# Kernel tuning notes

Measured on AMD Instinct MI355X. Metric: run time of the kernel, lower is better.

The kernel has to match this reference:

```python
import jax, jax.numpy as jnp
import numpy as np
import math

HIDDEN = 1024
NUM_HEADS = 16
HEAD_DIM = HIDDEN // NUM_HEADS
B, S = 4, 1024


def setup_inputs() -> dict:
    key = jax.random.key(0)
    ks = jax.random.split(key, 16)
    sd = 1.0 / math.sqrt(HIDDEN)
    inp = {
        "x": jax.random.normal(ks[0], (B, S, HIDDEN), jnp.float32),
        "spikes": jax.random.uniform(ks[1], (B, S, HIDDEN), jnp.float32),
        "membrane_potential": jax.random.normal(ks[2], (B, S, HIDDEN), jnp.float32),
        "Wq": jax.random.normal(ks[3], (HIDDEN, HIDDEN), jnp.float32) * sd,
        "bq": jnp.zeros((HIDDEN,), jnp.float32),
        "Wk": jax.random.normal(ks[4], (HIDDEN, HIDDEN), jnp.float32) * sd,
        "bk": jnp.zeros((HIDDEN,), jnp.float32),
        "Wv": jax.random.normal(ks[5], (HIDDEN, HIDDEN), jnp.float32) * sd,
        "bv": jnp.zeros((HIDDEN,), jnp.float32),
        "Wo": jax.random.normal(ks[6], (HIDDEN, HIDDEN), jnp.float32) * sd,
        "bo": jnp.zeros((HIDDEN,), jnp.float32),
        "tau_decay": jnp.ones((NUM_HEADS,), jnp.float32) * 10.0,
        "Wg": jax.random.normal(ks[7], (HIDDEN, 2 * HIDDEN), jnp.float32) * sd,
        "bg": jnp.zeros((HIDDEN,), jnp.float32),
    }
    return inp


def _heads(t):  # [B,S,H] -> [B,nH,S,hd]
    Bv, Sv, _ = t.shape
    return t.reshape(Bv, Sv, NUM_HEADS, HEAD_DIM).transpose(0, 2, 1, 3)


def reference(x, spikes, membrane_potential, Wq, bq, Wk, bk, Wv, bv, Wo, bo, tau_decay, Wg, bg):
    scale = 1.0 / math.sqrt(HEAD_DIM)
    q = _heads(x @ Wq.T + bq)
    k = _heads(x @ Wk.T + bk)
    v = _heads(x @ Wv.T + bv)

    # raw scores [B,nH,S,S]
    scores = jnp.einsum('bhqd,bhkd->bhqk', q, k) * scale

    # per-head exponential temporal decay mask [nH,S,S]
    times = jnp.arange(S, dtype=jnp.float32)
    tdiff = jnp.abs(times[:, None] - times[None, :])  # [S,S]
    tmask = jnp.exp(-tdiff[None] / tau_decay[:, None, None])
    scores = scores * tmask[None]

    # spike correlation term
    sm = _heads(spikes)
    spike_attn = jnp.einsum('bhqd,bhkd->bhqk', sm, sm) * scale
    scores = scores * (1.0 + spike_attn)

    # membrane gating of V
    v = v * jax.nn.sigmoid(_heads(membrane_potential))

    probs = jax.nn.softmax(scores, axis=-1)
    context = jnp.einsum('bhqk,bhkd->bhqd', probs, v)
    context = context.transpose(0, 2, 1, 3).reshape(B, S, HIDDEN)

    # dendritic gate
    gate_in = jnp.concatenate([context, membrane_potential], axis=-1)
    gate = jax.nn.sigmoid(gate_in @ Wg.T + bg)
    context = context * gate

    return context @ Wo.T + bo
```

## Files before the change

### kernel.cpp

```cpp
#include <hip/hip_runtime.h>
#include <math.h>
#include <stdint.h>

namespace {

typedef __attribute__((ext_vector_type(8))) short s8v;
typedef __attribute__((ext_vector_type(4))) float f4v;
typedef unsigned short u16;

__device__ __forceinline__ float fexp2(float x) {
  return __builtin_amdgcn_exp2f(x);
}

__device__ __forceinline__ u16 f2bf(float f) {
  union { float f; uint32_t u; } v; v.f = f;
  uint32_t r = v.u + 0x7fffu + ((v.u >> 16) & 1u);
  return (u16)(r >> 16);
}
__device__ __forceinline__ float bf2f(u16 h) {
  union { uint32_t u; float f; } v; v.u = ((uint32_t)h) << 16;
  return v.f;
}
__device__ __forceinline__ uint32_t pk2r(float a, float b) {
  return (uint32_t)f2bf(a) | ((uint32_t)f2bf(b) << 16);
}
__device__ __forceinline__ uint32_t pk2(float a, float b) {
  union { float f; uint32_t u; } x, y; x.f = a; y.f = b;
  return ((x.u + 0x8000u) >> 16) | ((y.u + 0x8000u) & 0xffff0000u);
}
__device__ __forceinline__ float sigmoidf_(float x) { return 1.0f / (1.0f + __expf(-x)); }

__device__ __forceinline__ void gload16(const u16* g, u16* l) {
  __builtin_amdgcn_global_load_lds(
      (const __attribute__((address_space(1))) void*)g,
      (__attribute__((address_space(3))) void*)l, 16, 0, 0);
}

struct CvtJob { const float* src; u16* dst; };
struct CvtArgs { CvtJob j[18]; float* vz; };

__global__ __launch_bounds__(256) void cvt_kernel(CvtArgs a) {
  if (blockIdx.y == 0 && blockIdx.x < 4) {
    float4 z; z.x = 0.f; z.y = 0.f; z.z = 0.f; z.w = 0.f;
    ((float4*)a.vz)[blockIdx.x * 256 + threadIdx.x] = z;
  }
  const CvtJob jb = a.j[blockIdx.y];
  const int i = blockIdx.x * 256 + threadIdx.x;
  const float4 v = ((const float4*)jb.src)[i];
  uint2 pk;
  pk.x = pk2r(v.x, v.y);
  pk.y = pk2r(v.z, v.w);
  ((uint2*)jb.dst)[i] = pk;
}

__global__ __launch_bounds__(256) void qkv_gemm(
    const u16* __restrict__ xb,
    const u16* __restrict__ Wqb, const u16* __restrict__ Wkb, const u16* __restrict__ Wvb,
    const float* __restrict__ bq, const float* __restrict__ bk, const float* __restrict__ bv,
    const float* __restrict__ mem,
    u16* __restrict__ Qb, u16* __restrict__ Kb, u16* __restrict__ Vt,
    float* __restrict__ Vtot) {
  __shared__ __align__(16) u16 as_[2][4096], bs_[2][4096];
  const int t = threadIdx.x;
  const int nb = blockIdx.x, mb = blockIdx.y;
  const int sel = nb >> 3;
  const u16* W = sel == 0 ? Wqb : (sel == 1 ? Wkb : Wvb);
  const float* bias = sel == 0 ? bq : (sel == 1 ? bk : bv);
  const int m0 = mb * 128, n0 = (nb & 7) * 128;
  const f4v fz = {0.f, 0.f, 0.f, 0.f};
  f4v acc[4][4];
#pragma unroll
  for (int i = 0; i < 4; ++i)
#pragma unroll
    for (int j = 0; j < 4; ++j) acc[i][j] = fz;

  const int l = t & 63, w = t >> 6, wm = w >> 1, wn = w & 1;
  const int lr = l & 15, lq = l >> 4;
  const int rh = lr >> 1;
  const int rb4 = (lr & 1) << 2;

  const int sc0 = (t & 7) ^ ((t >> 3) & 7);
  const int sgrow = ((t >> 3) << 1) + (sc0 >> 2);
  const int sgk = (sc0 & 3) << 3;

#define QKV_STAGE(k0, bsel)                                                    \
  {                                                                            \
    const int kk_ = (k0);                                                      \
    _Pragma("unroll") for (int u = 0; u < 2; ++u) {                            \
      gload16(xb + (size_t)(m0 + u * 64 + sgrow) * 1024 + kk_ + sgk,           \
              &as_[bsel][u * 2048 + t * 8]);                                   \
      gload16(W + (size_t)(n0 + u * 64 + sgrow) * 1024 + kk_ + sgk,            \
              &bs_[bsel][u * 2048 + t * 8]);                                   \
    }                                                                          \
  }

  QKV_STAGE(0, 0);
  QKV_STAGE(32, 1);
  asm volatile("s_waitcnt vmcnt(4)" ::: "memory");
  __builtin_amdgcn_s_barrier();

  if (sel < 2) {
    for (int c = 0; c < 32; ++c) {
      const int pp = c & 1;
      s8v af[4], bf[4];
#pragma unroll
      for (int mi = 0; mi < 4; ++mi)
        af[mi] = *(const s8v*)(&as_[pp][(wm * 32 + mi * 8 + rh) * 64 +
                                        (((rb4 + lq) ^ rh) * 8)]);
#pragma unroll
      for (int ni = 0; ni < 4; ++ni)
        bf[ni] = *(const s8v*)(&bs_[pp][(wn * 32 + ni * 8 + rh) * 64 +
                                        (((rb4 + lq) ^ rh) * 8)]);
      asm volatile("s_waitcnt lgkmcnt(0)" ::: "memory");
      __builtin_amdgcn_sched_barrier(0);
      __builtin_amdgcn_s_barrier();
      if (c + 2 < 32) QKV_STAGE((c + 2) << 5, pp);
      __builtin_amdgcn_s_setprio(1);
#pragma unroll
      for (int mi = 0; mi < 4; ++mi)
#pragma unroll
        for (int ni = 0; ni < 4; ++ni)
          acc[mi][ni] = __builtin_amdgcn_mfma_f32_16x16x32_bf16(
              bf[ni], af[mi], acc[mi][ni], 0, 0, 0);
      __builtin_amdgcn_s_setprio(0);
      if (c + 2 < 32) {
        asm volatile("s_waitcnt vmcnt(4)" ::: "memory");
      } else if (c + 1 < 32) {
        asm volatile("s_waitcnt vmcnt(0)" ::: "memory");
      }
      if (c + 1 < 32) __builtin_amdgcn_s_barrier();
    }
    __builtin_amdgcn_sched_barrier(0);
    u16* dst = (sel == 0) ? Qb : Kb;
#pragma unroll
    for (int mi = 0; mi < 4; ++mi)
#pragma unroll
      for (int ni = 0; ni < 4; ++ni) {
        const int m = m0 + wm * 64 + mi * 16 + lr;
        const int nb4 = n0 + wn * 64 + ni * 16 + lq * 4;
        const float4 b4 = *(const float4*)&bias[nb4];
        uint2 pk;
        pk.x = pk2r(acc[mi][ni][0] + b4.x, acc[mi][ni][1] + b4.y);
        pk.y = pk2r(acc[mi][ni][2] + b4.z, acc[mi][ni][3] + b4.w);
        *(uint2*)(dst + (size_t)m * 1024 + nb4) = pk;
      }
  } else {
    for (int c = 0; c < 32; ++c) {
      const int pp = c & 1;
      s8v af[4], bf[4];
#pragma unroll
      for (int mi = 0; mi < 4; ++mi)
        af[mi] = *(const s8v*)(&as_[pp][(wm * 32 + mi * 8 + rh) * 64 +
                                        (((rb4 + lq) ^ rh) * 8)]);
#pragma unroll
      for (int ni = 0; ni < 4; ++ni)
        bf[ni] = *(const s8v*)(&bs_[pp][(wn * 32 + ni * 8 + rh) * 64 +
                                        (((rb4 + lq) ^ rh) * 8)]);
      asm volatile("s_waitcnt lgkmcnt(0)" ::: "memory");
      __builtin_amdgcn_sched_barrier(0);
      __builtin_amdgcn_s_barrier();
      if (c + 2 < 32) QKV_STAGE((c + 2) << 5, pp);
      __builtin_amdgcn_s_setprio(1);
#pragma unroll
      for (int mi = 0; mi < 4; ++mi)
#pragma unroll
        for (int ni = 0; ni < 4; ++ni)
          acc[mi][ni] = __builtin_amdgcn_mfma_f32_16x16x32_bf16(
              af[mi], bf[ni], acc[mi][ni], 0, 0, 0);
      __builtin_amdgcn_s_setprio(0);
      if (c + 2 < 32) {
        asm volatile("s_waitcnt vmcnt(4)" ::: "memory");
      } else if (c + 1 < 32) {
        asm volatile("s_waitcnt vmcnt(0)" ::: "memory");
      }
      if (c + 1 < 32) __builtin_amdgcn_s_barrier();
    }
    __builtin_amdgcn_sched_barrier(0);
    const int b = m0 >> 10;
    float vpart[4] = {0.f, 0.f, 0.f, 0.f};
#pragma unroll
    for (int mi = 0; mi < 4; ++mi)
#pragma unroll
      for (int ni = 0; ni < 4; ++ni) {
        const int mrow = m0 + wm * 64 + mi * 16 + lq * 4;
        const int ncol = n0 + wn * 64 + ni * 16 + lr;
        const int h = ncol >> 6, d = ncol & 63;
        const float bi = bias[ncol];
        float tv[4];
#pragma unroll
        for (int r = 0; r < 4; ++r)
          tv[r] = (acc[mi][ni][r] + bi) * sigmoidf_(mem[(size_t)(mrow + r) * 1024 + ncol]);
        vpart[ni] += (tv[0] + tv[1]) + (tv[2] + tv[3]);
        const int s = mrow & 1023;
        uint2 pk;
        pk.x = pk2r(tv[0], tv[1]);
        pk.y = pk2r(tv[2], tv[3]);
        *(uint2*)(Vt + ((size_t)((b * 16 + h) * 64 + d)) * 1024 + s) = pk;
      }
#pragma unroll
    for (int ni = 0; ni < 4; ++ni) {
      const int ncol = n0 + wn * 64 + ni * 16 + lr;
      atomicAdd(&Vtot[(size_t)(b * 16 + (ncol >> 6)) * 64 + (ncol & 63)], vpart[ni]);
    }
  }
#undef QKV_STAGE
}

template <int MODE>
__global__ __launch_bounds__(256) void gemm64(
    const u16* __restrict__ Ab, const u16* __restrict__ A2b,
    const u16* __restrict__ W, const float* __restrict__ bias,
    u16* __restrict__ outb, float* __restrict__ outf, int K) {
  __shared__ __align__(16) u16 as_[8192], bs_[16384];
  const int t = threadIdx.x, l = t & 63, w = t >> 6;
  const int wm = w >> 1, wn = w & 1, lr = l & 15, lq = l >> 4;
  const int m0 = blockIdx.y * 64, n0 = blockIdx.x * 128;
  const f4v fz = {0.f, 0.f, 0.f, 0.f};
  f4v acc[2][4];
#pragma unroll
  for (int i = 0; i < 2; ++i)
#pragma unroll
    for (int j = 0; j < 4; ++j) acc[i][j] = fz;
  const int rx = lr & 7;
  const int srow = t >> 3;
  const int scol = ((t & 7) ^ (srow & 7)) * 8;
  const int nc = K >> 6;

#define G64_STAGE(k0, bsel)                                                    \
  {                                                                            \
    const int kk_ = (k0);                                                      \
    const u16* Ae_ = Ab;                                                       \
    int ka_ = kk_;                                                             \
    if (MODE == 1 && kk_ >= 1024) { Ae_ = A2b; ka_ = kk_ - 1024; }             \
    _Pragma("unroll") for (int u = 0; u < 2; ++u)                              \
        gload16(Ae_ + (size_t)(m0 + u * 32 + srow) * 1024 + ka_ + scol,        \
                as_ + (bsel) * 4096 + u * 2048 + t * 8);                       \
    _Pragma("unroll") for (int u = 0; u < 4; ++u)                              \
        gload16(W + (size_t)(n0 + u * 32 + srow) * K + kk_ + scol,             \
                bs_ + (bsel) * 8192 + u * 2048 + t * 8);                       \
  }

  G64_STAGE(0, 0);
  G64_STAGE(64, 1);
  asm volatile("s_waitcnt vmcnt(6)" ::: "memory");
  __builtin_amdgcn_s_barrier();

  for (int c = 0; c < nc; ++c) {
    const int pp = c & 1;
    const int loA = pp * 4096, loB = pp * 8192;
    s8v af[2][2], bf[2][4];
#pragma unroll
    for (int ks = 0; ks < 2; ++ks) {
      const int co = ((ks * 4 + lq) ^ rx) * 8;
#pragma unroll
      for (int mi = 0; mi < 2; ++mi)
        af[ks][mi] = *(const s8v*)(as_ + loA + (wm * 32 + mi * 16 + lr) * 64 + co);
#pragma unroll
      for (int ni = 0; ni < 4; ++ni)
        bf[ks][ni] = *(const s8v*)(bs_ + loB + (wn * 64 + ni * 16 + lr) * 64 + co);
    }
    asm volatile("s_waitcnt lgkmcnt(0)" ::: "memory");
    __builtin_amdgcn_sched_barrier(0);
    __builtin_amdgcn_s_barrier();
    if (c + 2 < nc) G64_STAGE((c + 2) << 6, pp);
    __builtin_amdgcn_s_setprio(1);
#pragma unroll
    for (int ks = 0; ks < 2; ++ks)
#pragma unroll
      for (int mi = 0; mi < 2; ++mi)
#pragma unroll
        for (int ni = 0; ni < 4; ++ni)
          acc[mi][ni] = __builtin_amdgcn_mfma_f32_16x16x32_bf16(
              bf[ks][ni], af[ks][mi], acc[mi][ni], 0, 0, 0);
    __builtin_amdgcn_s_setprio(0);
    if (c + 2 < nc) {
      asm volatile("s_waitcnt vmcnt(6)" ::: "memory");
    } else if (c + 1 < nc) {
      asm volatile("s_waitcnt vmcnt(0)" ::: "memory");
    }
    if (c + 1 < nc) __builtin_amdgcn_s_barrier();
  }
  __builtin_amdgcn_sched_barrier(0);
#undef G64_STAGE

#pragma unroll
  for (int mi = 0; mi < 2; ++mi)
#pragma unroll
    for (int ni = 0; ni < 4; ++ni) {
      const int m = m0 + wm * 32 + mi * 16 + lr;
      const int nb4 = n0 + wn * 64 + ni * 16 + lq * 4;
      const float4 b4 = *(const float4*)&bias[nb4];
      if (MODE == 0) {
        float4 o;
        o.x = acc[mi][ni][0] + b4.x; o.y = acc[mi][ni][1] + b4.y;
        o.z = acc[mi][ni][2] + b4.z; o.w = acc[mi][ni][3] + b4.w;
        *(float4*)(outf + (size_t)m * 1024 + nb4) = o;
      } else {
        const uint2 a2 = *(const uint2*)(Ab + (size_t)m * 1024 + nb4);
        float cx[4] = {bf2f((u16)(a2.x & 0xffff)), bf2f((u16)(a2.x >> 16)),
                       bf2f((u16)(a2.y & 0xffff)), bf2f((u16)(a2.y >> 16))};
        float g[4];
        g[0] = cx[0] * sigmoidf_(acc[mi][ni][0] + b4.x);
        g[1] = cx[1] * sigmoidf_(acc[mi][ni][1] + b4.y);
        g[2] = cx[2] * sigmoidf_(acc[mi][ni][2] + b4.z);
        g[3] = cx[3] * sigmoidf_(acc[mi][ni][3] + b4.w);
        uint2 pk;
        pk.x = pk2r(g[0], g[1]);
        pk.y = pk2r(g[2], g[3]);
        *(uint2*)(outb + (size_t)m * 1024 + nb4) = pk;
      }
    }
}

__global__ __launch_bounds__(256) void attn_mfma(
    const u16* __restrict__ Qb, const u16* __restrict__ Kb,
    const u16* __restrict__ SPb, const u16* __restrict__ Vt,
    const float* __restrict__ tau, const float* __restrict__ Vtot,
    u16* __restrict__ CTXb) {
  __shared__ u16 kbuf[4096], skbuf[4096], vbuf[4096];
  __shared__ u16 pbuf[4][16 * 64];
  const int t = threadIdx.x, l = t & 63, w = t >> 6;
  const int lr = l & 15, lq = l >> 4;
  const int p = blockIdx.x;
  const int g = (p & 7) + 8 * (p >> 7);
  const int qt = (p >> 3) & 15;
  const int h = g & 15, b = g >> 4;

  const float tv_ = tau[h];
  const float c2 = 1.44269504088896f / tv_;
  const float K0 = 0.125f * 1.44269504088896f;
  int rad = (int)ceilf(tv_ * 0.171875f);
  if (rad > 15) rad = 15;
  const int jlo = (qt - rad < 0) ? 0 : qt - rad;
  const int jhi = (qt + rad > 15) ? 15 : qt + rad;
  const int farCnt = 16 - (jhi - jlo + 1);

  float cN[4], cNi[4], cR[4], cRi[4];
#pragma unroll
  for (int i = 0; i < 4; ++i) {
    cN[i]  = fexp2(c2 * (float)(i * 16));
    cNi[i] = fexp2(-c2 * (float)(i * 16));
    cR[i]  = fexp2(c2 * (float)(lq * 4 + i));
    cRi[i] = fexp2(-c2 * (float)(lq * 4 + i));
  }

  s8v qf[2], sf[2];
  {
    const size_t base = ((size_t)(b * 1024 + qt * 64 + w * 16 + lr)) * 1024 + h * 64 + lq * 8;
    qf[0] = *(const s8v*)(Qb + base);
    qf[1] = *(const s8v*)(Qb + base + 32);
    sf[0] = *(const s8v*)(SPb + base);
    sf[1] = *(const s8v*)(SPb + base + 32);
  }
  const s8v ones = {0x3F80, 0x3F80, 0x3F80, 0x3F80, 0x3F80, 0x3F80, 0x3F80, 0x3F80};

  const f4v fz = {0.f, 0.f, 0.f, 0.f};
  f4v oacc[4], vs[4];
  float lacc[4];
#pragma unroll
  for (int i = 0; i < 4; ++i) { oacc[i] = fz; vs[i] = fz; lacc[i] = 0.f; }

  const int iqw = qt * 64 + w * 16;
  const int srow = t >> 3;
  const int csw = ((t & 7) ^ (srow & 7)) * 8;
  const int rx = lr & 7;
  u16* pw = pbuf[w];

  for (int jc = jlo; jc <= jhi; ++jc) {
    const int j0 = jc * 64;
    __syncthreads();
    {
      const size_t kg = ((size_t)(b * 1024 + j0 + srow)) * 1024 + h * 64 + csw;
      gload16(Kb + kg, kbuf + t * 8);
      gload16(Kb + kg + 32 * 1024, kbuf + 2048 + t * 8);
      gload16(SPb + kg, skbuf + t * 8);
      gload16(SPb + kg + 32 * 1024, skbuf + 2048 + t * 8);
      const size_t vg = ((size_t)((b * 16 + h) * 64 + srow)) * 1024 + j0 + csw;
      gload16(Vt + vg, vbuf + t * 8);
      gload16(Vt + vg + 32 * 1024, vbuf + 2048 + t * 8);
    }
    __syncthreads();

    f4v sa[4], ssa[4];
#pragma unroll
    for (int ni = 0; ni < 4; ++ni) { sa[ni] = fz; ssa[ni] = fz; }
#pragma unroll
    for (int ks = 0; ks < 2; ++ks) {
#pragma unroll
      for (int ni = 0; ni < 4; ++ni) {
        const int off = (ni * 16 + lr) * 64 + (((ks * 4 + lq) ^ rx) * 8);
        const s8v kf = *(const s8v*)(kbuf + off);
        sa[ni] = __builtin_amdgcn_mfma_f32_16x16x32_bf16(kf, qf[ks], sa[ni], 0, 0, 0);
        const s8v skf = *(const s8v*)(skbuf + off);
        ssa[ni] = __builtin_amdgcn_mfma_f32_16x16x32_bf16(skf, sf[ks], ssa[ni], 0, 0, 0);
      }
    }

    const int D0 = iqw - j0;
    float pv[4][4];
    if (jc < qt) {
      const float EA = K0 * fexp2(-c2 * (float)(D0 + lr));
#pragma unroll
      for (int ni = 0; ni < 4; ++ni)
#pragma unroll
        for (int r = 0; r < 4; ++r) {
          const float t1 = fmaf(ssa[ni][r], 0.125f, 1.0f);
          const float e = fexp2(sa[ni][r] * cN[ni] * cR[r] * EA * t1);
          pv[ni][r] = e;
          lacc[ni] += e;
        }
    } else if (jc > qt) {
      const float EAi = K0 * fexp2(c2 * (float)(D0 + lr));
#pragma unroll
      for (int ni = 0; ni < 4; ++ni)
#pragma unroll
        for (int r = 0; r < 4; ++r) {
          const float t1 = fmaf(ssa[ni][r], 0.125f, 1.0f);
          const float e = fexp2(sa[ni][r] * cNi[ni] * cRi[r] * EAi * t1);
          pv[ni][r] = e;
          lacc[ni] += e;
        }
    } else {
      const float EA  = K0 * fexp2(-c2 * (float)(D0 + lr));
      const float EAi = K0 * fexp2(c2 * (float)(D0 + lr));
#pragma unroll
      for (int ni = 0; ni < 4; ++ni)
#pragma unroll
        for (int r = 0; r < 4; ++r) {
          const int jloc = ni * 16 + lq * 4 + r;
          const float fb = cN[ni] * cR[r] * EA;
          const float fa = cNi[ni] * cRi[r] * EAi;
          const float f = (D0 + lr >= jloc) ? fb : fa;
          const float t1 = fmaf(ssa[ni][r], 0.125f, 1.0f);
          const float e = fexp2(sa[ni][r] * f * t1);
          pv[ni][r] = e;
          lacc[ni] += e;
        }
    }

#pragma unroll
    for (int ni = 0; ni < 4; ++ni) {
      const int phys = (ni * 2 + (lq >> 1)) ^ rx;
      uint2 p2;
      p2.x = pk2(pv[ni][0], pv[ni][1]);
      p2.y = pk2(pv[ni][2], pv[ni][3]);
      *(uint2*)(pw + lr * 64 + phys * 8 + (lq & 1) * 4) = p2;
    }

#pragma unroll
    for (int ks = 0; ks < 2; ++ks) {
      const s8v pf = *(const s8v*)(pw + lr * 64 + (((ks * 4 + lq) ^ rx) * 8));
#pragma unroll
      for (int nd = 0; nd < 4; ++nd) {
        const int off = (nd * 16 + lr) * 64 + (((ks * 4 + lq) ^ rx) * 8);
        const s8v vf = *(const s8v*)(vbuf + off);
        oacc[nd] = __builtin_amdgcn_mfma_f32_16x16x32_bf16(vf, pf, oacc[nd], 0, 0, 0);
        vs[nd] = __builtin_amdgcn_mfma_f32_16x16x32_bf16(vf, ones, vs[nd], 0, 0, 0);
      }
    }
  }

  float ls = (lacc[0] + lacc[1]) + (lacc[2] + lacc[3]);
  ls += __shfl_xor(ls, 16);
  ls += __shfl_xor(ls, 32);
  ls += 64.0f * (float)farCnt;
  const float inv = 1.0f / ls;
  const float* vt0 = Vtot + (size_t)(b * 16 + h) * 64;
  const size_t orow = ((size_t)(b * 1024 + qt * 64 + w * 16 + lr)) * 1024 + h * 64;
#pragma unroll
  for (int nd = 0; nd < 4; ++nd) {
    const float4 vt4 = *(const float4*)(vt0 + nd * 16 + lq * 4);
    float o0 = (oacc[nd][0] + vt4.x - vs[nd][0]) * inv;
    float o1 = (oacc[nd][1] + vt4.y - vs[nd][1]) * inv;
    float o2 = (oacc[nd][2] + vt4.z - vs[nd][2]) * inv;
    float o3 = (oacc[nd][3] + vt4.w - vs[nd][3]) * inv;
    uint2 o;
    o.x = pk2r(o0, o1);
    o.y = pk2r(o2, o3);
    *(uint2*)(CTXb + orow + nd * 16 + lq * 4) = o;
  }
}

}

extern "C" void kernel_launch(void* const* d_in, const int* in_sizes, int n_in,
                              void* d_out, int out_size, void* d_ws, size_t ws_size,
                              hipStream_t stream) {
  const float* x      = (const float*)d_in[0];
  const float* spikes = (const float*)d_in[1];
  const float* mem    = (const float*)d_in[2];
  const float* Wq     = (const float*)d_in[3];
  const float* bq     = (const float*)d_in[4];
  const float* Wk     = (const float*)d_in[5];
  const float* bk     = (const float*)d_in[6];
  const float* Wv     = (const float*)d_in[7];
  const float* bv     = (const float*)d_in[8];
  const float* Wo     = (const float*)d_in[9];
  const float* bo     = (const float*)d_in[10];
  const float* tau    = (const float*)d_in[11];
  const float* Wg     = (const float*)d_in[12];
  const float* bg     = (const float*)d_in[13];
  float* out = (float*)d_out;

  uint8_t* w8 = (uint8_t*)d_ws;
  u16* spb  = (u16*)(w8);
  u16* xb   = (u16*)(w8 + (8u << 20));
  u16* Wqb  = (u16*)(w8 + (16u << 20));
  u16* Wkb  = (u16*)(w8 + (18u << 20));
  u16* Wvb  = (u16*)(w8 + (20u << 20));
  u16* Wob  = (u16*)(w8 + (22u << 20));
  u16* Wgb  = (u16*)(w8 + (24u << 20));
  u16* Qb   = (u16*)(w8 + (28u << 20));
  u16* Kb   = (u16*)(w8 + (36u << 20));
  u16* Vt   = (u16*)(w8 + (44u << 20));
  u16* CTXb = (u16*)(w8 + (52u << 20));
  float* Vtot = (float*)(w8 + (60u << 20));
  u16* memb = (u16*)d_out;
  u16* gctx = xb;

  constexpr size_t QE = 262144 * 4;
  CvtArgs ca;
  for (int q = 0; q < 4; ++q) ca.j[q]     = {x + q * QE,      xb + q * QE};
  for (int q = 0; q < 4; ++q) ca.j[4 + q] = {spikes + q * QE, spb + q * QE};
  for (int q = 0; q < 4; ++q) ca.j[8 + q] = {mem + q * QE,    memb + q * QE};
  ca.j[12] = {Wq, Wqb};
  ca.j[13] = {Wk, Wkb};
  ca.j[14] = {Wv, Wvb};
  ca.j[15] = {Wo, Wob};
  ca.j[16] = {Wg, Wgb};
  ca.j[17] = {Wg + QE, Wgb + QE};
  ca.vz = Vtot;
  cvt_kernel<<<dim3(1024, 18), 256, 0, stream>>>(ca);

  qkv_gemm<<<dim3(24, 32), 256, 0, stream>>>(xb, Wqb, Wkb, Wvb, bq, bk, bv, mem,
                                             Qb, Kb, Vt, Vtot);
  attn_mfma<<<dim3(1024), 256, 0, stream>>>(Qb, Kb, spb, Vt, tau, Vtot, CTXb);
  gemm64<1><<<dim3(8, 64), 256, 0, stream>>>(CTXb, memb, Wgb, bg, gctx, nullptr, 2048);
  gemm64<0><<<dim3(8, 64), 256, 0, stream>>>(gctx, nullptr, Wob, bo, nullptr, out, 1024);
}
```

Baseline: 255.7 us.

## Fuse Q/K/V projections into one block sharing the x tile

The QKV GEMM now has each 512-thread block compute Q, K and V for the same 128x128 output tile, so the x tile in shared memory is loaded once and reused across all three weight matrices instead of being fetched by three separate blocks. Software pipelining is deepened from double to quad buffering with adjusted vmcnt waits. The grid shrinks from 768 to 256 blocks, which cuts redundant activation traffic but lowers block-level parallelism and raises shared memory use, and may affect occupancy.

```diff
diff --git a/kernel.cpp b/kernel.cpp
--- a/kernel.cpp
+++ b/kernel.cpp
@@ -53,143 +53,140 @@
   ((uint2*)jb.dst)[i] = pk;
 }
 
-__global__ __launch_bounds__(256) void qkv_gemm(
+__global__ __launch_bounds__(512, 2) void qkv_gemm(
     const u16* __restrict__ xb,
     const u16* __restrict__ Wqb, const u16* __restrict__ Wkb, const u16* __restrict__ Wvb,
     const float* __restrict__ bq, const float* __restrict__ bk, const float* __restrict__ bv,
     const float* __restrict__ mem,
     u16* __restrict__ Qb, u16* __restrict__ Kb, u16* __restrict__ Vt,
     float* __restrict__ Vtot) {
-  __shared__ __align__(16) u16 as_[2][4096], bs_[2][4096];
+  __shared__ __align__(16) u16 as_[4][4096];
+  __shared__ __align__(16) u16 bs_[4][12288];
   const int t = threadIdx.x;
   const int nb = blockIdx.x, mb = blockIdx.y;
-  const int sel = nb >> 3;
-  const u16* W = sel == 0 ? Wqb : (sel == 1 ? Wkb : Wvb);
-  const float* bias = sel == 0 ? bq : (sel == 1 ? bk : bv);
-  const int m0 = mb * 128, n0 = (nb & 7) * 128;
-  const f4v fz = {0.f, 0.f, 0.f, 0.f};
-  f4v acc[4][4];
-#pragma unroll
-  for (int i = 0; i < 4; ++i)
-#pragma unroll
-    for (int j = 0; j < 4; ++j) acc[i][j] = fz;
-
-  const int l = t & 63, w = t >> 6, wm = w >> 1, wn = w & 1;
+  const int m0 = mb * 128, n0 = nb * 128;
+  const int l = t & 63, w = t >> 6;
+  const int wm = w >> 2, wn = w & 3;
   const int lr = l & 15, lq = l >> 4;
   const int rh = lr >> 1;
   const int rb4 = (lr & 1) << 2;
 
-  const int sc0 = (t & 7) ^ ((t >> 3) & 7);
-  const int sgrow = ((t >> 3) << 1) + (sc0 >> 2);
+  const f4v fz = {0.f, 0.f, 0.f, 0.f};
+  f4v aq[4][2], ak[4][2], av[4][2];
+#pragma unroll
+  for (int i = 0; i < 4; ++i)
+#pragma unroll
+    for (int j = 0; j < 2; ++j) { aq[i][j] = fz; ak[i][j] = fz; av[i][j] = fz; }
+
+  const int tt = t & 255, uu = t >> 8;
+  const int sc0 = (tt & 7) ^ ((tt >> 3) & 7);
+  const int sgrow = ((tt >> 3) << 1) + (sc0 >> 2);
   const int sgk = (sc0 & 3) << 3;
 
-#define QKV_STAGE(k0, bsel)                                                    \
+  const u16* ga = xb + (size_t)(m0 + uu * 64 + sgrow) * 1024 + sgk;
+  const u16* gq = Wqb + (size_t)(n0 + uu * 64 + sgrow) * 1024 + sgk;
+  const u16* gk = Wkb + (size_t)(n0 + uu * 64 + sgrow) * 1024 + sgk;
+  const u16* gv = Wvb + (size_t)(n0 + uu * 64 + sgrow) * 1024 + sgk;
+  const int lofs = uu * 2048 + tt * 8;
+
+#define QKV_STAGE(c)                                                           \
   {                                                                            \
-    const int kk_ = (k0);                                                      \
-    _Pragma("unroll") for (int u = 0; u < 2; ++u) {                            \
-      gload16(xb + (size_t)(m0 + u * 64 + sgrow) * 1024 + kk_ + sgk,           \
-              &as_[bsel][u * 2048 + t * 8]);                                   \
-      gload16(W + (size_t)(n0 + u * 64 + sgrow) * 1024 + kk_ + sgk,            \
-              &bs_[bsel][u * 2048 + t * 8]);                                   \
-    }                                                                          \
-  }
-
-  QKV_STAGE(0, 0);
-  QKV_STAGE(32, 1);
-  asm volatile("s_waitcnt vmcnt(4)" ::: "memory");
+    const int ko_ = (c) * 32;                                                  \
+    const int bb_ = (c) & 3;                                                   \
+    gload16(ga + ko_, &as_[bb_][lofs]);                                        \
+    gload16(gq + ko_, &bs_[bb_][lofs]);                                        \
+    gload16(gk + ko_, &bs_[bb_][4096 + lofs]);                                 \
+    gload16(gv + ko_, &bs_[bb_][8192 + lofs]);                                 \
+  }
+
+  QKV_STAGE(0); QKV_STAGE(1); QKV_STAGE(2); QKV_STAGE(3);
+  asm volatile("s_waitcnt vmcnt(12)" ::: "memory");
   __builtin_amdgcn_s_barrier();
 
-  if (sel < 2) {
-    for (int c = 0; c < 32; ++c) {
-      const int pp = c & 1;
-      s8v af[4], bf[4];
-#pragma unroll
-      for (int mi = 0; mi < 4; ++mi)
-        af[mi] = *(const s8v*)(&as_[pp][(wm * 32 + mi * 8 + rh) * 64 +
-                                        (((rb4 + lq) ^ rh) * 8)]);
-#pragma unroll
-      for (int ni = 0; ni < 4; ++ni)
-        bf[ni] = *(const s8v*)(&bs_[pp][(wn * 32 + ni * 8 + rh) * 64 +
-                                        (((rb4 + lq) ^ rh) * 8)]);
-      asm volatile("s_waitcnt lgkmcnt(0)" ::: "memory");
-      __builtin_amdgcn_sched_barrier(0);
-      __builtin_amdgcn_s_barrier();
-      if (c + 2 < 32) QKV_STAGE((c + 2) << 5, pp);
-      __builtin_amdgcn_s_setprio(1);
-#pragma unroll
-      for (int mi = 0; mi < 4; ++mi)
-#pragma unroll
-        for (int ni = 0; ni < 4; ++ni)
-          acc[mi][ni] = __builtin_amdgcn_mfma_f32_16x16x32_bf16(
-              bf[ni], af[mi], acc[mi][ni], 0, 0, 0);
-      __builtin_amdgcn_s_setprio(0);
-      if (c + 2 < 32) {
-        asm volatile("s_waitcnt vmcnt(4)" ::: "memory");
-      } else if (c + 1 < 32) {
-        asm volatile("s_waitcnt vmcnt(0)" ::: "memory");
+  const int co = ((rb4 + lq) ^ rh) * 8;
+  for (int c = 0; c < 32; ++c) {
+    const int cb = c & 3;
+    s8v af[4], bfq[2], bfk[2], bfv[2];
+#pragma unroll
+    for (int mi = 0; mi < 4; ++mi)
+      af[mi] = *(const s8v*)(&as_[cb][(wm * 32 + mi * 8 + rh) * 64 + co]);
+#pragma unroll
+    for (int ni = 0; ni < 2; ++ni) {
+      const int ro = (wn * 16 + ni * 8 + rh) * 64 + co;
+      bfq[ni] = *(const s8v*)(&bs_[cb][ro]);
+      bfk[ni] = *(const s8v*)(&bs_[cb][4096 + ro]);
+      bfv[ni] = *(const s8v*)(&bs_[cb][8192 + ro]);
+    }
+    asm volatile("s_waitcnt lgkmcnt(0)" ::: "memory");
+    __builtin_amdgcn_sched_barrier(0);
+    __builtin_amdgcn_s_barrier();
+    if (c + 4 < 32) QKV_STAGE(c + 4);
+    __builtin_amdgcn_s_setprio(1);
+#pragma unroll
+    for (int mi = 0; mi < 4; ++mi)
+#pragma unroll
+      for (int ni = 0; ni < 2; ++ni) {
+        aq[mi][ni] = __builtin_amdgcn_mfma_f32_16x16x32_bf16(
+            bfq[ni], af[mi], aq[mi][ni], 0, 0, 0);
+        ak[mi][ni] = __builtin_amdgcn_mfma_f32_16x16x32_bf16(
+            bfk[ni], af[mi], ak[mi][ni], 0, 0, 0);
+        av[mi][ni] = __builtin_amdgcn_mfma_f32_16x16x32_bf16(
+            af[mi], bfv[ni], av[mi][ni], 0, 0, 0);
       }
-      if (c + 1 < 32) __builtin_amdgcn_s_barrier();
-    }
-    __builtin_amdgcn_sched_barrier(0);
-    u16* dst = (sel == 0) ? Qb : Kb;
+    __builtin_amdgcn_s_setprio(0);
+    if (c < 28) {
+      asm volatile("s_waitcnt vmcnt(12)" ::: "memory");
+    } else if (c == 28) {
+      asm volatile("s_waitcnt vmcnt(8)" ::: "memory");
+    } else if (c == 29) {
+      asm volatile("s_waitcnt vmcnt(4)" ::: "memory");
+    } else if (c == 30) {
+      asm volatile("s_waitcnt vmcnt(0)" ::: "memory");
+    }
+    if (c < 31) __builtin_amdgcn_s_barrier();
+  }
+#undef QKV_STAGE
+  __builtin_amdgcn_sched_barrier(0);
+
+#pragma unroll
+  for (int mi = 0; mi < 4; ++mi)
+#pragma unroll
+    for (int ni = 0; ni < 2; ++ni) {
+      const int m = m0 + wm * 64 + mi * 16 + lr;
+      const int nb4 = n0 + wn * 32 + ni * 16 + lq * 4;
+      const float4 b4 = *(const float4*)&bq[nb4];
+      uint2 pk;
+      pk.x = pk2r(aq[mi][ni][0] + b4.x, aq[mi][ni][1] + b4.y);
+      pk.y = pk2r(aq[mi][ni][2] + b4.z, aq[mi][ni][3] + b4.w);
+      *(uint2*)(Qb + (size_t)m * 1024 + nb4) = pk;
+    }
+#pragma unroll
+  for (int mi = 0; mi < 4; ++mi)
+#pragma unroll
+    for (int ni = 0; ni < 2; ++ni) {
+      const int m = m0 + wm * 64 + mi * 16 + lr;
+      const int nb4 = n0 + wn * 32 + ni * 16 + lq * 4;
+      const float4 b4 = *(const float4*)&bk[nb4];
+      uint2 pk;
+      pk.x = pk2r(ak[mi][ni][0] + b4.x, ak[mi][ni][1] + b4.y);
+      pk.y = pk2r(ak[mi][ni][2] + b4.z, ak[mi][ni][3] + b4.w);
+      *(uint2*)(Kb + (size_t)m * 1024 + nb4) = pk;
+    }
+  {
+    const int b = m0 >> 10;
+    float vpart[2] = {0.f, 0.f};
 #pragma unroll
     for (int mi = 0; mi < 4; ++mi)
 #pragma unroll
-      for (int ni = 0; ni < 4; ++ni) {
-        const int m = m0 + wm * 64 + mi * 16 + lr;
-        const int nb4 = n0 + wn * 64 + ni * 16 + lq * 4;
-        const float4 b4 = *(const float4*)&bias[nb4];
-        uint2 pk;
-        pk.x = pk2r(acc[mi][ni][0] + b4.x, acc[mi][ni][1] + b4.y);
-        pk.y = pk2r(acc[mi][ni][2] + b4.z, acc[mi][ni][3] + b4.w);
-        *(uint2*)(dst + (size_t)m * 1024 + nb4) = pk;
-      }
-  } else {
-    for (int c = 0; c < 32; ++c) {
-      const int pp = c & 1;
-      s8v af[4], bf[4];
-#pragma unroll
-      for (int mi = 0; mi < 4; ++mi)
-        af[mi] = *(const s8v*)(&as_[pp][(wm * 32 + mi * 8 + rh) * 64 +
-                                        (((rb4 + lq) ^ rh) * 8)]);
-#pragma unroll
-      for (int ni = 0; ni < 4; ++ni)
-        bf[ni] = *(const s8v*)(&bs_[pp][(wn * 32 + ni * 8 + rh) * 64 +
-                                        (((rb4 + lq) ^ rh) * 8)]);
-      asm volatile("s_waitcnt lgkmcnt(0)" ::: "memory");
-      __builtin_amdgcn_sched_barrier(0);
-      __builtin_amdgcn_s_barrier();
-      if (c + 2 < 32) QKV_STAGE((c + 2) << 5, pp);
-      __builtin_amdgcn_s_setprio(1);
-#pragma unroll
-      for (int mi = 0; mi < 4; ++mi)
-#pragma unroll
-        for (int ni = 0; ni < 4; ++ni)
-          acc[mi][ni] = __builtin_amdgcn_mfma_f32_16x16x32_bf16(
-              af[mi], bf[ni], acc[mi][ni], 0, 0, 0);
-      __builtin_amdgcn_s_setprio(0);
-      if (c + 2 < 32) {
-        asm volatile("s_waitcnt vmcnt(4)" ::: "memory");
-      } else if (c + 1 < 32) {
-        asm volatile("s_waitcnt vmcnt(0)" ::: "memory");
-      }
-      if (c + 1 < 32) __builtin_amdgcn_s_barrier();
-    }
-    __builtin_amdgcn_sched_barrier(0);
-    const int b = m0 >> 10;
-    float vpart[4] = {0.f, 0.f, 0.f, 0.f};
-#pragma unroll
-    for (int mi = 0; mi < 4; ++mi)
-#pragma unroll
-      for (int ni = 0; ni < 4; ++ni) {
+      for (int ni = 0; ni < 2; ++ni) {
         const int mrow = m0 + wm * 64 + mi * 16 + lq * 4;
-        const int ncol = n0 + wn * 64 + ni * 16 + lr;
+        const int ncol = n0 + wn * 32 + ni * 16 + lr;
         const int h = ncol >> 6, d = ncol & 63;
-        const float bi = bias[ncol];
+        const float bi = bv[ncol];
         float tv[4];
 #pragma unroll
         for (int r = 0; r < 4; ++r)
-          tv[r] = (acc[mi][ni][r] + bi) * sigmoidf_(mem[(size_t)(mrow + r) * 1024 + ncol]);
+          tv[r] = (av[mi][ni][r] + bi) * sigmoidf_(mem[(size_t)(mrow + r) * 1024 + ncol]);
         vpart[ni] += (tv[0] + tv[1]) + (tv[2] + tv[3]);
         const int s = mrow & 1023;
         uint2 pk;
@@ -198,12 +195,11 @@
         *(uint2*)(Vt + ((size_t)((b * 16 + h) * 64 + d)) * 1024 + s) = pk;
       }
 #pragma unroll
-    for (int ni = 0; ni < 4; ++ni) {
-      const int ncol = n0 + wn * 64 + ni * 16 + lr;
+    for (int ni = 0; ni < 2; ++ni) {
+      const int ncol = n0 + wn * 32 + ni * 16 + lr;
       atomicAdd(&Vtot[(size_t)(b * 16 + (ncol >> 6)) * 64 + (ncol & 63)], vpart[ni]);
     }
   }
-#undef QKV_STAGE
 }
 
 template <int MODE>
@@ -532,8 +528,8 @@
   ca.vz = Vtot;
   cvt_kernel<<<dim3(1024, 18), 256, 0, stream>>>(ca);
 
-  qkv_gemm<<<dim3(24, 32), 256, 0, stream>>>(xb, Wqb, Wkb, Wvb, bq, bk, bv, mem,
-                                             Qb, Kb, Vt, Vtot);
+  qkv_gemm<<<dim3(8, 32), 512, 0, stream>>>(xb, Wqb, Wkb, Wvb, bq, bk, bv, mem,
+                                            Qb, Kb, Vt, Vtot);
   attn_mfma<<<dim3(1024), 256, 0, stream>>>(Qb, Kb, spb, Vt, tau, Vtot, CTXb);
   gemm64<1><<<dim3(8, 64), 256, 0, stream>>>(CTXb, memb, Wgb, bg, gctx, nullptr, 2048);
   gemm64<0><<<dim3(8, 64), 256, 0, stream>>>(gctx, nullptr, Wob, bo, nullptr, out, 1024);
```

Measured after the change: 248.3 us. 2.9% less time.
